# Kernel optimization log

Hardware: AMD Instinct MI355X
Metric: run time of the kernel (lower is better)

The kernel has to match this reference:

```python
import jax, jax.numpy as jnp
import numpy as np

QMIN, QMAX = -128.0, 127.0


def _quant_dequant_act_8bit(x):
    # Dynamic per-row asymmetric 8-bit quantization of activations, then dequant.
    xmin = jnp.min(x, axis=-1, keepdims=True)
    xmax = jnp.max(x, axis=-1, keepdims=True)
    scale = jnp.maximum((xmax - xmin) / 255.0, 1e-8)
    zp = jnp.clip(jnp.round(QMIN - xmin / scale), QMIN, QMAX)
    qx = jnp.clip(jnp.round(x / scale) + zp, QMIN, QMAX)
    return (qx - zp) * scale


def setup_inputs() -> dict:
    key = jax.random.key(0)
    k_x, k_w, k_s, k_b = jax.random.split(key, 4)
    m, k, n, group_size = 32, 8192, 14336, 128
    n_groups = k // group_size  # 64
    x = jax.random.normal(k_x, (m, k), dtype=jnp.float32)
    # unsigned 4-bit codes in [0, 16); dequant uses (q - 8) * scale
    q_weight = jax.random.randint(k_w, (n, k), 0, 16, dtype=jnp.int32)
    w_scale = jax.random.uniform(k_s, (n, n_groups), dtype=jnp.float32) * 0.01 + 1e-3
    bias = jax.random.normal(k_b, (n,), dtype=jnp.float32) * 0.02
    return {"x": x, "q_weight": q_weight, "w_scale": w_scale, "bias": bias, "group_size": group_size}


def reference(x, q_weight, w_scale, bias, group_size):
    # _linear_8bit_act_4bit_weight: int8-act x 4-bit group-quantized weight GEMM + bias
    m, k = x.shape
    n = q_weight.shape[0]
    g = k // group_size
    x_dq = _quant_dequant_act_8bit(x).reshape(m, g, group_size)          # [m, g, gs]
    qw = (q_weight.astype(jnp.float32) - 8.0).reshape(n, g, group_size)  # [n, g, gs]
    # per-group partial products, then apply group scales and reduce over groups
    partial = jnp.einsum("mgc,ngc->mng", x_dq, qw)                        # [m, n, g]
    out = jnp.einsum("mng,ng->mn", partial, w_scale)                      # [m, n]
    return out + bias
```

## Files before the change

### kernel.cpp

```cpp
#include <hip/hip_runtime.h>
#include <hip/hip_bf16.h>

#define Mdim 32
#define Kdim 8192
#define Ndim 14336
#define GSZ  128
#define NGRP 64

#define KB 8
#define KC (Kdim/KB)
#define BN 64

typedef __attribute__((ext_vector_type(16))) float f32x16;
typedef __attribute__((ext_vector_type(8)))  short bf16x8;
typedef __attribute__((ext_vector_type(4)))  int   i32x4;

__global__ __launch_bounds__(256) void quant_rows_kernel(
        const float* __restrict__ x,
        const float* __restrict__ bias,
        __hip_bfloat16* __restrict__ xq,
        float* __restrict__ scales,
        float* __restrict__ out) {
    const int row = blockIdx.x;
    const float4* __restrict__ xr4 = (const float4*)(x + (size_t)row * Kdim);

    float lmin = 3.4e38f, lmax = -3.4e38f;
#pragma unroll
    for (int i = 0; i < Kdim / 4 / 256; ++i) {
        const float4 v = xr4[threadIdx.x + i * 256];
        lmin = fminf(lmin, fminf(fminf(v.x, v.y), fminf(v.z, v.w)));
        lmax = fmaxf(lmax, fmaxf(fmaxf(v.x, v.y), fmaxf(v.z, v.w)));
    }
#pragma unroll
    for (int off = 32; off > 0; off >>= 1) {
        lmin = fminf(lmin, __shfl_xor(lmin, off, 64));
        lmax = fmaxf(lmax, __shfl_xor(lmax, off, 64));
    }
    __shared__ float smin[4], smax[4];
    const int wid = threadIdx.x >> 6;
    if ((threadIdx.x & 63) == 0) { smin[wid] = lmin; smax[wid] = lmax; }
    __syncthreads();
    const float xmin = fminf(fminf(smin[0], smin[1]), fminf(smin[2], smin[3]));
    const float xmax = fmaxf(fmaxf(smax[0], smax[1]), fmaxf(smax[2], smax[3]));

    const float scale = fmaxf((xmax - xmin) / 255.0f, 1e-8f);
    float zp = rintf(-128.0f - xmin / scale);
    zp = fminf(fmaxf(zp, -128.0f), 127.0f);
    if (threadIdx.x == 0) scales[row] = scale;

    ushort4* __restrict__ xq4 = (ushort4*)(xq + (size_t)row * Kdim);
#pragma unroll
    for (int i = 0; i < Kdim / 4 / 256; ++i) {
        const float4 v = xr4[threadIdx.x + i * 256];
        ushort4 o;
        float q;
        q = fminf(fmaxf(rintf(v.x / scale) + zp, -128.0f), 127.0f);
        o.x = __bfloat16_as_ushort(__float2bfloat16(q - zp));
        q = fminf(fmaxf(rintf(v.y / scale) + zp, -128.0f), 127.0f);
        o.y = __bfloat16_as_ushort(__float2bfloat16(q - zp));
        q = fminf(fmaxf(rintf(v.z / scale) + zp, -128.0f), 127.0f);
        o.z = __bfloat16_as_ushort(__float2bfloat16(q - zp));
        q = fminf(fmaxf(rintf(v.w / scale) + zp, -128.0f), 127.0f);
        o.w = __bfloat16_as_ushort(__float2bfloat16(q - zp));
        xq4[threadIdx.x + i * 256] = o;
    }

    const float4* __restrict__ b4 = (const float4*)bias;
    float4* __restrict__ o4 = (float4*)(out + (size_t)row * Ndim);
#pragma unroll
    for (int i = 0; i < Ndim / 4 / 256; ++i)
        o4[threadIdx.x + i * 256] = b4[threadIdx.x + i * 256];
}

__global__ __launch_bounds__(128) void qlin_main_kernel(
        const int* __restrict__ qw, const float* __restrict__ wscale,
        const __hip_bfloat16* __restrict__ xq, const float* __restrict__ scales,
        float* __restrict__ out) {
    const int lane  = threadIdx.x & 63;
    const int wid   = threadIdx.x >> 6;
    const int col   = blockIdx.x * BN + wid * 32 + (lane & 31);
    const int k0    = blockIdx.y * KC;
    const int khalf = (lane >> 5) * 8;

    const int* __restrict__ wp = qw + (size_t)col * Kdim + k0 + khalf;
    const __hip_bfloat16* __restrict__ ap =
        xq + (size_t)(lane & 31) * Kdim + k0 + khalf;
    const float* __restrict__ wsp = wscale + (size_t)col * NGRP + (k0 / GSZ);

    f32x16 acc = {};

    for (int g = 0; g < KC / GSZ; ++g) {
        const float ws   = wsp[g];
        const float m8ws = -8.0f * ws;
        const int* __restrict__ wpg = wp + g * GSZ;
        const __hip_bfloat16* __restrict__ apg = ap + g * GSZ;
#pragma unroll
        for (int s = 0; s < GSZ / 16; ++s) {
            const i32x4 q0 = *(const i32x4*)(wpg + s * 16);
            const i32x4 q1 = *(const i32x4*)(wpg + s * 16 + 4);
            const bf16x8 a = *(const bf16x8*)(apg + s * 16);

            union { bf16x8 v; __hip_bfloat162 h[4]; } bu;
            const float f0 = fmaf((float)q0[0], ws, m8ws);
            const float f1 = fmaf((float)q0[1], ws, m8ws);
            const float f2 = fmaf((float)q0[2], ws, m8ws);
            const float f3 = fmaf((float)q0[3], ws, m8ws);
            const float f4 = fmaf((float)q1[0], ws, m8ws);
            const float f5 = fmaf((float)q1[1], ws, m8ws);
            const float f6 = fmaf((float)q1[2], ws, m8ws);
            const float f7 = fmaf((float)q1[3], ws, m8ws);
            bu.h[0] = __float22bfloat162_rn(float2{f0, f1});
            bu.h[1] = __float22bfloat162_rn(float2{f2, f3});
            bu.h[2] = __float22bfloat162_rn(float2{f4, f5});
            bu.h[3] = __float22bfloat162_rn(float2{f6, f7});

            acc = __builtin_amdgcn_mfma_f32_32x32x16_bf16(a, bu.v, acc, 0, 0, 0);
        }
    }

    const int rbase = (lane >> 5) * 4;
    const float4 s0 = *(const float4*)(scales + rbase);
    const float4 s1 = *(const float4*)(scales + rbase + 8);
    const float4 s2 = *(const float4*)(scales + rbase + 16);
    const float4 s3 = *(const float4*)(scales + rbase + 24);
    const float sr[16] = {s0.x, s0.y, s0.z, s0.w, s1.x, s1.y, s1.z, s1.w,
                          s2.x, s2.y, s2.z, s2.w, s3.x, s3.y, s3.z, s3.w};
#pragma unroll
    for (int r = 0; r < 16; ++r) {
        const int row = (r & 3) + 8 * (r >> 2) + rbase;
        unsafeAtomicAdd(out + (size_t)row * Ndim + col, sr[r] * acc[r]);
    }
}

extern "C" void kernel_launch(void* const* d_in, const int* in_sizes, int n_in,
                              void* d_out, int out_size, void* d_ws, size_t ws_size,
                              hipStream_t stream) {
    const float* x    = (const float*)d_in[0];
    const int*   qw   = (const int*)d_in[1];
    const float* wsc  = (const float*)d_in[2];
    const float* bias = (const float*)d_in[3];
    float* out = (float*)d_out;

    float* scales = (float*)d_ws;
    __hip_bfloat16* xq = (__hip_bfloat16*)((char*)d_ws + 256);

    quant_rows_kernel<<<Mdim, 256, 0, stream>>>(x, bias, xq, scales, out);
    qlin_main_kernel<<<dim3(Ndim / BN, KB), 128, 0, stream>>>(qw, wsc, xq, scales, out);
}
```

Baseline: 635.0 us.

## Replace atomic split-K accumulation with partial buffers and a separate reduce kernel

Each split-K slice now writes its accumulator tile to its own partial buffer with nontemporal stores instead of atomically adding into the output. A new reduce kernel sums the eight partials, applies the per-row activation scale and adds the bias, so the bias initialisation leaves the quantisation kernel. This removes atomic contention and read-modify-write traffic on the output. In exchange it adds a third launch and writes and reads about 14 MB of partials.

New measurement: 650.8 us. +2.5%, slower.

```diff
diff --git a/kernel.cpp b/kernel.cpp
--- a/kernel.cpp
+++ b/kernel.cpp
@@ -17,10 +17,8 @@
 
 __global__ __launch_bounds__(256) void quant_rows_kernel(
         const float* __restrict__ x,
-        const float* __restrict__ bias,
         __hip_bfloat16* __restrict__ xq,
-        float* __restrict__ scales,
-        float* __restrict__ out) {
+        float* __restrict__ scales) {
     const int row = blockIdx.x;
     const float4* __restrict__ xr4 = (const float4*)(x + (size_t)row * Kdim);
 
@@ -64,18 +62,12 @@
         o.w = __bfloat16_as_ushort(__float2bfloat16(q - zp));
         xq4[threadIdx.x + i * 256] = o;
     }
-
-    const float4* __restrict__ b4 = (const float4*)bias;
-    float4* __restrict__ o4 = (float4*)(out + (size_t)row * Ndim);
-#pragma unroll
-    for (int i = 0; i < Ndim / 4 / 256; ++i)
-        o4[threadIdx.x + i * 256] = b4[threadIdx.x + i * 256];
 }
 
 __global__ __launch_bounds__(128) void qlin_main_kernel(
         const int* __restrict__ qw, const float* __restrict__ wscale,
-        const __hip_bfloat16* __restrict__ xq, const float* __restrict__ scales,
-        float* __restrict__ out) {
+        const __hip_bfloat16* __restrict__ xq,
+        float* __restrict__ partials) {
     const int lane  = threadIdx.x & 63;
     const int wid   = threadIdx.x >> 6;
     const int col   = blockIdx.x * BN + wid * 32 + (lane & 31);
@@ -118,18 +110,37 @@
         }
     }
 
+    float* __restrict__ pp =
+        partials + ((size_t)blockIdx.y * Mdim) * Ndim + col;
     const int rbase = (lane >> 5) * 4;
-    const float4 s0 = *(const float4*)(scales + rbase);
-    const float4 s1 = *(const float4*)(scales + rbase + 8);
-    const float4 s2 = *(const float4*)(scales + rbase + 16);
-    const float4 s3 = *(const float4*)(scales + rbase + 24);
-    const float sr[16] = {s0.x, s0.y, s0.z, s0.w, s1.x, s1.y, s1.z, s1.w,
-                          s2.x, s2.y, s2.z, s2.w, s3.x, s3.y, s3.z, s3.w};
 #pragma unroll
     for (int r = 0; r < 16; ++r) {
         const int row = (r & 3) + 8 * (r >> 2) + rbase;
-        unsafeAtomicAdd(out + (size_t)row * Ndim + col, sr[r] * acc[r]);
+        __builtin_nontemporal_store(acc[r], pp + (size_t)row * Ndim);
     }
+}
+
+__global__ __launch_bounds__(256) void reduce_kernel(
+        const float* __restrict__ partials, const float* __restrict__ scales,
+        const float* __restrict__ bias, float* __restrict__ out) {
+    const int n4 = blockIdx.x * 256 + threadIdx.x;
+    const int m  = blockIdx.y;
+    const size_t row4 = (size_t)m * (Ndim / 4) + n4;
+
+    float4 s = {0.f, 0.f, 0.f, 0.f};
+#pragma unroll
+    for (int ky = 0; ky < KB; ++ky) {
+        const float4 p = ((const float4*)partials)[(size_t)ky * Mdim * (Ndim / 4) + row4];
+        s.x += p.x; s.y += p.y; s.z += p.z; s.w += p.w;
+    }
+    const float sc = scales[m];
+    const float4 b = ((const float4*)bias)[n4];
+    float4 o;
+    o.x = fmaf(sc, s.x, b.x);
+    o.y = fmaf(sc, s.y, b.y);
+    o.z = fmaf(sc, s.z, b.z);
+    o.w = fmaf(sc, s.w, b.w);
+    ((float4*)out)[row4] = o;
 }
 
 extern "C" void kernel_launch(void* const* d_in, const int* in_sizes, int n_in,
@@ -143,7 +154,9 @@
 
     float* scales = (float*)d_ws;
     __hip_bfloat16* xq = (__hip_bfloat16*)((char*)d_ws + 256);
+    float* partials = (float*)((char*)d_ws + (1u << 20));
 
-    quant_rows_kernel<<<Mdim, 256, 0, stream>>>(x, bias, xq, scales, out);
-    qlin_main_kernel<<<dim3(Ndim / BN, KB), 128, 0, stream>>>(qw, wsc, xq, scales, out);
+    quant_rows_kernel<<<Mdim, 256, 0, stream>>>(x, xq, scales);
+    qlin_main_kernel<<<dim3(Ndim / BN, KB), 128, 0, stream>>>(qw, wsc, xq, partials);
+    reduce_kernel<<<dim3(Ndim / 4 / 256, Mdim), 256, 0, stream>>>(partials, scales, bias, out);
 }
```

## Double-buffer weight tiles into LDS via direct global-to-LDS loads

Applied to the files above, without the earlier changes.

The main GEMM kernel now streams each warp's int32 weight tile through a double-buffered shared-memory ring, filled with global_load_lds DMA into an XOR-swizzled layout. The next tile's loads and activation fragments are issued before the current tile is computed, with manual vmcnt waits. Per-group weight scales are loaded up front as float4 vectors. The aim is to hide global latency on the memory-bound weight stream and coalesce row-wise loads, at the cost of added LDS use, hand-tuned wait counts that must match the number of outstanding loads, and possible swizzle or bank-conflict problems.

New measurement: 629.0 us. About the same (-0.9%).

```diff
diff --git a/kernel.cpp b/kernel.cpp
--- a/kernel.cpp
+++ b/kernel.cpp
@@ -9,11 +9,16 @@
 
 #define KB 8
 #define KC (Kdim/KB)
+#define BK 64
+#define NT (KC/BK)
 #define BN 64
 
 typedef __attribute__((ext_vector_type(16))) float f32x16;
 typedef __attribute__((ext_vector_type(8)))  short bf16x8;
 typedef __attribute__((ext_vector_type(4)))  int   i32x4;
+
+typedef __attribute__((address_space(1))) const int gint_t;
+typedef __attribute__((address_space(3))) int       lint_t;
 
 __global__ __launch_bounds__(256) void quant_rows_kernel(
         const float* __restrict__ x,
@@ -76,49 +81,104 @@
         const int* __restrict__ qw, const float* __restrict__ wscale,
         const __hip_bfloat16* __restrict__ xq, const float* __restrict__ scales,
         float* __restrict__ out) {
-    const int lane  = threadIdx.x & 63;
-    const int wid   = threadIdx.x >> 6;
-    const int col   = blockIdx.x * BN + wid * 32 + (lane & 31);
-    const int k0    = blockIdx.y * KC;
-    const int khalf = (lane >> 5) * 8;
-
-    const int* __restrict__ wp = qw + (size_t)col * Kdim + k0 + khalf;
+    __shared__ int ldsw[2][2][32 * BK];
+
+    const int lane   = threadIdx.x & 63;
+    const int wid    = threadIdx.x >> 6;
+    const int col31  = lane & 31;
+    const int hi     = lane >> 5;
+    const int colbase = blockIdx.x * BN + wid * 32;
+    const int col     = colbase + col31;
+    const int k0      = blockIdx.y * KC;
+
+    const int r_dma = lane >> 4;
+    const int c_dma = lane & 15;
+
     const __hip_bfloat16* __restrict__ ap =
-        xq + (size_t)(lane & 31) * Kdim + k0 + khalf;
+        xq + (size_t)col31 * Kdim + k0 + hi * 8;
     const float* __restrict__ wsp = wscale + (size_t)col * NGRP + (k0 / GSZ);
 
+    const float4 wv0 = *(const float4*)(wsp);
+    const float4 wv1 = *(const float4*)(wsp + 4);
+    const float wsf[8] = {wv0.x, wv0.y, wv0.z, wv0.w,
+                          wv1.x, wv1.y, wv1.z, wv1.w};
+
     f32x16 acc = {};
-
-    for (int g = 0; g < KC / GSZ; ++g) {
-        const float ws   = wsp[g];
+    bf16x8 af[2][4];
+
+#pragma unroll
+    for (int j = 0; j < 8; ++j) {
+        const int r = 4 * j + r_dma;
+        const int g = c_dma ^ (r & 15);
+        const int* src = qw + (size_t)(colbase + r) * Kdim + k0 + g * 4;
+        __builtin_amdgcn_global_load_lds((gint_t*)src,
+                                         (lint_t*)&ldsw[0][wid][j * 256],
+                                         16, 0, 0);
+    }
+#pragma unroll
+    for (int s = 0; s < 4; ++s)
+        af[0][s] = *(const bf16x8*)(ap + s * 16);
+
+    const int swz = (col31 & 15) << 4;
+
+#pragma unroll
+    for (int gI = 0; gI < 8; ++gI) {
+        const float ws   = wsf[gI];
         const float m8ws = -8.0f * ws;
-        const int* __restrict__ wpg = wp + g * GSZ;
-        const __hip_bfloat16* __restrict__ apg = ap + g * GSZ;
-#pragma unroll
-        for (int s = 0; s < GSZ / 16; ++s) {
-            const i32x4 q0 = *(const i32x4*)(wpg + s * 16);
-            const i32x4 q1 = *(const i32x4*)(wpg + s * 16 + 4);
-            const bf16x8 a = *(const bf16x8*)(apg + s * 16);
-
-            union { bf16x8 v; __hip_bfloat162 h[4]; } bu;
-            const float f0 = fmaf((float)q0[0], ws, m8ws);
-            const float f1 = fmaf((float)q0[1], ws, m8ws);
-            const float f2 = fmaf((float)q0[2], ws, m8ws);
-            const float f3 = fmaf((float)q0[3], ws, m8ws);
-            const float f4 = fmaf((float)q1[0], ws, m8ws);
-            const float f5 = fmaf((float)q1[1], ws, m8ws);
-            const float f6 = fmaf((float)q1[2], ws, m8ws);
-            const float f7 = fmaf((float)q1[3], ws, m8ws);
-            bu.h[0] = __float22bfloat162_rn(float2{f0, f1});
-            bu.h[1] = __float22bfloat162_rn(float2{f2, f3});
-            bu.h[2] = __float22bfloat162_rn(float2{f4, f5});
-            bu.h[3] = __float22bfloat162_rn(float2{f6, f7});
-
-            acc = __builtin_amdgcn_mfma_f32_32x32x16_bf16(a, bu.v, acc, 0, 0, 0);
+#pragma unroll
+        for (int h = 0; h < 2; ++h) {
+            const int t = gI * 2 + h;
+            if (t < NT - 1) {
+                const int nt = t + 1;
+                const int nb = nt & 1;
+#pragma unroll
+                for (int j = 0; j < 8; ++j) {
+                    const int r = 4 * j + r_dma;
+                    const int g = c_dma ^ (r & 15);
+                    const int* src = qw + (size_t)(colbase + r) * Kdim
+                                     + k0 + nt * BK + g * 4;
+                    __builtin_amdgcn_global_load_lds(
+                        (gint_t*)src, (lint_t*)&ldsw[nb][wid][j * 256], 16, 0, 0);
+                }
+#pragma unroll
+                for (int s = 0; s < 4; ++s)
+                    af[nb][s] = *(const bf16x8*)(ap + nt * BK + s * 16);
+                asm volatile("s_waitcnt vmcnt(12)" ::: "memory");
+            } else {
+                asm volatile("s_waitcnt vmcnt(0)" ::: "memory");
+            }
+            __builtin_amdgcn_sched_barrier(0);
+
+            const int cb = t & 1;
+            const char* wbase =
+                (const char*)&ldsw[cb][wid][0] + col31 * (BK * 4);
+#pragma unroll
+            for (int s = 0; s < 4; ++s) {
+                const int b0 = ((s << 6) | (hi << 5)) ^ swz;
+                const i32x4 q0 = *(const i32x4*)(wbase + b0);
+                const i32x4 q1 = *(const i32x4*)(wbase + (b0 ^ 16));
+
+                union { bf16x8 v; __hip_bfloat162 h2[4]; } bu;
+                const float f0 = fmaf((float)q0[0], ws, m8ws);
+                const float f1 = fmaf((float)q0[1], ws, m8ws);
+                const float f2 = fmaf((float)q0[2], ws, m8ws);
+                const float f3 = fmaf((float)q0[3], ws, m8ws);
+                const float f4 = fmaf((float)q1[0], ws, m8ws);
+                const float f5 = fmaf((float)q1[1], ws, m8ws);
+                const float f6 = fmaf((float)q1[2], ws, m8ws);
+                const float f7 = fmaf((float)q1[3], ws, m8ws);
+                bu.h2[0] = __float22bfloat162_rn(float2{f0, f1});
+                bu.h2[1] = __float22bfloat162_rn(float2{f2, f3});
+                bu.h2[2] = __float22bfloat162_rn(float2{f4, f5});
+                bu.h2[3] = __float22bfloat162_rn(float2{f6, f7});
+
+                acc = __builtin_amdgcn_mfma_f32_32x32x16_bf16(
+                    af[cb][s], bu.v, acc, 0, 0, 0);
+            }
         }
     }
 
-    const int rbase = (lane >> 5) * 4;
+    const int rbase = hi * 4;
     const float4 s0 = *(const float4*)(scales + rbase);
     const float4 s1 = *(const float4*)(scales + rbase + 8);
     const float4 s2 = *(const float4*)(scales + rbase + 16);
```
